# Kernel tuning notes

Measured on AMD Instinct MI355X. Metric: run time of the kernel, lower is better.

## Reference

```python
import jax, jax.numpy as jnp
import numpy as np

B, S, D, H = 2, 2048, 1024, 16
HD = D // H

def setup_inputs() -> dict:
    key = jax.random.key(0)
    k1, k2, k3 = jax.random.split(key, 3)
    x = jax.random.normal(k1, (B, S, D), dtype=jnp.float32)
    c_attn_w = jax.random.normal(k2, (D, 3 * D), dtype=jnp.float32) * 0.02
    c_attn_b = jnp.zeros((3 * D,), dtype=jnp.float32)
    c_proj_w = jax.random.normal(k3, (D, D), dtype=jnp.float32) * 0.02
    c_proj_b = jnp.zeros((D,), dtype=jnp.float32)
    return {"x": x, "c_attn_w": c_attn_w, "c_attn_b": c_attn_b,
            "c_proj_w": c_proj_w, "c_proj_b": c_proj_b}

def reference(x, c_attn_w, c_attn_b, c_proj_w, c_proj_b):
    bsz, seq_len, d = x.shape
    # Conv1D: addmm(bias, x, weight) -> x @ W + b
    qkv = x @ c_attn_w + c_attn_b                      # [B,S,3D]
    xq, xk, xv = jnp.split(qkv, 3, axis=-1)
    # [B,H,S,hd]
    xq = xq.reshape(bsz, seq_len, H, HD).transpose(0, 2, 1, 3)
    xk = xk.reshape(bsz, seq_len, H, HD).transpose(0, 2, 1, 3)
    xv = xv.reshape(bsz, seq_len, H, HD).transpose(0, 2, 1, 3)
    # Eager attention: QK^T / sqrt(hd), causal mask, softmax, AV
    scale = jnp.asarray(HD, x.dtype) ** 0.5
    attn_weights = jnp.einsum('bhqd,bhkd->bhqk', xq, xk) / scale
    causal = jnp.tril(jnp.ones((seq_len, seq_len), dtype=bool))
    mask_value = jnp.finfo(attn_weights.dtype).min
    attn_weights = jnp.where(causal[None, None], attn_weights, mask_value)
    attn_weights = jax.nn.softmax(attn_weights, axis=-1)
    attn_output = jnp.einsum('bhqk,bhkd->bhqd', attn_weights, xv)  # [B,H,S,hd]
    attn_output = attn_output.transpose(0, 2, 1, 3).reshape(bsz, seq_len, d)
    attn_output = attn_output @ c_proj_w + c_proj_b
    return attn_output
```

## Files before the change

### kernel.cpp

```cpp
#include <hip/hip_runtime.h>
#include <hip/hip_bf16.h>
#include <stdint.h>

#define S_LEN 2048
#define D_DIM 1024
#define N_HEAD 16

typedef unsigned short u16;
typedef __attribute__((ext_vector_type(4))) float f32x4;
typedef __attribute__((ext_vector_type(16))) float f32x16;
typedef __attribute__((ext_vector_type(8))) short bf16x8;
typedef __attribute__((ext_vector_type(4))) unsigned short u16x4;
typedef __attribute__((ext_vector_type(8))) unsigned short u16x8;
typedef __attribute__((ext_vector_type(4))) float flt4;

#define MFMA16(a, b, c) __builtin_amdgcn_mfma_f32_16x16x32_bf16((a), (b), (c), 0, 0, 0)
#define MFMA32(a, b, c) __builtin_amdgcn_mfma_f32_32x32x16_bf16((a), (b), (c), 0, 0, 0)

__device__ __forceinline__ u16 f32_bf16(float f) {
    union { float f; uint32_t u; } x;
    x.f = f;
    uint32_t r = (x.u + 0x7FFFu + ((x.u >> 16) & 1u)) >> 16;
    return (u16)r;
}

__device__ __forceinline__ uint32_t pack2(float a, float b) {
    __hip_bfloat162 h = __float22bfloat162_rn(float2{a, b});
    return *(uint32_t*)&h;
}

__device__ __forceinline__ void gload_lds16(const void* g, void* l) {
    __builtin_amdgcn_global_load_lds(
        (const __attribute__((address_space(1))) unsigned int*)(uintptr_t)g,
        (__attribute__((address_space(3))) unsigned int*)(uint32_t)(uintptr_t)l,
        16, 0, 0);
}


__global__ __launch_bounds__(256) void cvt_bf16_kernel(const float* __restrict__ in,
                                                       u16* __restrict__ out, int n) {
    int i = (blockIdx.x * 256 + threadIdx.x) * 4;
    if (i < n) {
        flt4 v = *(const flt4*)(in + i);
        u16x4 u;
        u[0] = f32_bf16(v[0]); u[1] = f32_bf16(v[1]);
        u[2] = f32_bf16(v[2]); u[3] = f32_bf16(v[3]);
        *(u16x4*)(out + i) = u;
    }
}

__global__ __launch_bounds__(256) void transpose_cvt_kernel(const float* __restrict__ in,
                                                            u16* __restrict__ out,
                                                            int R, int C) {
    __shared__ float tile[32][33];
    int tc = blockIdx.x * 32, tr = blockIdx.y * 32;
    int lx = threadIdx.x & 31, ly = threadIdx.x >> 5;
#pragma unroll
    for (int i = 0; i < 32; i += 8)
        tile[ly + i][lx] = in[(size_t)(tr + ly + i) * C + tc + lx];
    __syncthreads();
#pragma unroll
    for (int i = 0; i < 32; i += 8)
        out[(size_t)(tc + ly + i) * R + tr + lx] = f32_bf16(tile[lx][ly + i]);
}

__global__ __launch_bounds__(256) void v_transpose_kernel(const u16* __restrict__ Vin,
                                                          u16* __restrict__ Vt) {
    __shared__ u16 tile[64][72];
    const int bh = blockIdx.y, st = blockIdx.x;
    const int t = threadIdx.x;
    const u16* src = Vin + ((size_t)bh * S_LEN + st * 64) * 64;
    const int r = t >> 3, c = (t & 7) * 8;
#pragma unroll
    for (int i = 0; i < 2; i++) {
        int rr = r + i * 32;
        *(u16x8*)&tile[rr][c] = *(const u16x8*)(src + rr * 64 + c);
    }
    __syncthreads();
    const int d = t & 63, sc = t >> 6;
    u16x8 o0, o1;
#pragma unroll
    for (int j = 0; j < 8; j++) o0[j] = tile[sc * 16 + j][d];
#pragma unroll
    for (int j = 0; j < 8; j++) o1[j] = tile[sc * 16 + 8 + j][d];
    u16* dst = Vt + ((size_t)bh * 64 + d) * S_LEN + st * 64 + sc * 16;
    *(u16x8*)dst = o0;
    *(u16x8*)(dst + 8) = o1;
}


template <int MODE>
__global__ __launch_bounds__(256)
void gemm_bt_kernel(const u16* __restrict__ A, const u16* __restrict__ Bt,
                    const float* __restrict__ bias,
                    float* __restrict__ outF,
                    u16* __restrict__ qo, u16* __restrict__ ko, u16* __restrict__ vo,
                    int M, int N, int K) {
    __shared__ u16 As[128 * 32];
    __shared__ u16 Bs[128 * 32];
    const int tid = threadIdx.x;
    const int w = tid >> 6, lane = tid & 63;
    const int lr = lane & 15, lg = lane >> 4;
    const int gx = gridDim.x;
    const int nwg = gx * gridDim.y;
    const int wg = blockIdx.y * gx + blockIdx.x;
    const int swz = (wg & 7) * (nwg >> 3) + (wg >> 3);
    const int bm = (swz / gx) * 128, bn = (swz % gx) * 128;
    const int wr = w >> 1, wc = w & 1;

    f32x4 acc[4][4];
#pragma unroll
    for (int m = 0; m < 4; m++)
#pragma unroll
        for (int n = 0; n < 4; n++) acc[m][n] = (f32x4){0.f, 0.f, 0.f, 0.f};

    const u16* Abase = A + (size_t)(bm + (tid >> 2)) * K + (tid & 3) * 8;
    const u16* Bbase = Bt + (size_t)(bn + (tid >> 2)) * K + (tid & 3) * 8;
    u16* AsW = As + w * 512;
    u16* BsW = Bs + w * 512;

    for (int kt = 0; kt < K; kt += 32) {
        gload_lds16(Abase + kt, AsW);
        gload_lds16(Abase + kt + (size_t)64 * K, AsW + 2048);
        gload_lds16(Bbase + kt, BsW);
        gload_lds16(Bbase + kt + (size_t)64 * K, BsW + 2048);
        __syncthreads();

        bf16x8 a[4], b[4];
        const bf16x8* Av = (const bf16x8*)As;
        const bf16x8* Bv = (const bf16x8*)Bs;
#pragma unroll
        for (int m = 0; m < 4; m++) a[m] = Av[(wr * 64 + m * 16 + lr) * 4 + lg];
#pragma unroll
        for (int n = 0; n < 4; n++) b[n] = Bv[(wc * 64 + n * 16 + lr) * 4 + lg];
#pragma unroll
        for (int m = 0; m < 4; m++)
#pragma unroll
            for (int n = 0; n < 4; n++)
                acc[m][n] = MFMA16(a[m], b[n], acc[m][n]);
        __syncthreads();
    }

    const int rowb = bm + wr * 64, colb = bn + wc * 64;
    if (MODE == 0) {
#pragma unroll
        for (int m = 0; m < 4; m++)
#pragma unroll
            for (int j = 0; j < 4; j++) {
                int r = rowb + m * 16 + lg * 4 + j;
                size_t base = (size_t)r * N;
#pragma unroll
                for (int n = 0; n < 4; n++) {
                    int c = colb + n * 16 + lr;
                    outF[base + c] = acc[m][n][j] + bias[c];
                }
            }
    } else {
        const int part = colb >> 10;
        const int ccb = colb & (D_DIM - 1);
        u16* dst = (part == 0) ? qo : (part == 1) ? ko : vo;
        const float scale = (part == 0) ? 0.125f * 1.44269504f : 1.f;
#pragma unroll
        for (int m = 0; m < 4; m++)
#pragma unroll
            for (int j = 0; j < 4; j++) {
                int r = rowb + m * 16 + lg * 4 + j;
                int bb = r >> 11, s = r & (S_LEN - 1);
#pragma unroll
                for (int n = 0; n < 4; n++) {
                    int c = colb + n * 16 + lr;
                    int cc = ccb + n * 16 + lr;
                    int h = cc >> 6, d = cc & 63;
                    float v = (acc[m][n][j] + bias[c]) * scale;
                    dst[((size_t)(bb * N_HEAD + h) * S_LEN + s) * 64 + d] = f32_bf16(v);
                }
            }
    }
}


__global__ __launch_bounds__(128, 2)
void flash_attn_kernel(const u16* __restrict__ Qg, const u16* __restrict__ Kg,
                       const u16* __restrict__ Vt, u16* __restrict__ Og) {
    const int id = blockIdx.x;
    const int bh = id & 31;
    const int p  = id >> 5;
    const int w = threadIdx.x >> 6;
    const int lane = threadIdx.x & 63;
    const int ql = lane & 31, hi = lane >> 5;
    const int qbA = p * 32, qbB = (63 - p) * 32;
    const int last = 63 - p;

    const u16* Qh = Qg + (size_t)bh * S_LEN * 64;
    const u16* Kh = Kg + (size_t)bh * S_LEN * 64;
    const u16* Vh = Vt + (size_t)bh * 64 * S_LEN;

    __shared__ float mbuf[2][64][34];

    bf16x8 qfA[4], qfB[4];
#pragma unroll
    for (int c = 0; c < 4; c++) {
        qfA[c] = *(const bf16x8*)(Qh + (size_t)(qbA + ql) * 64 + c * 16 + hi * 8);
        qfB[c] = *(const bf16x8*)(Qh + (size_t)(qbB + ql) * 64 + c * 16 + hi * 8);
    }

    f32x16 otA0 = {}, otA1 = {}, otB0 = {}, otB1 = {};
    float mA = -1e30f, lA = 0.f, mB = -1e30f, lB = 0.f;

    auto loadKV = [&](int t, bf16x8 (&k)[4], bf16x8 (&v)[4]) {
        const u16* kp = Kh + ((size_t)t * 32 + ql) * 64 + hi * 8;
#pragma unroll
        for (int c = 0; c < 4; c++) k[c] = *(const bf16x8*)(kp + c * 16);
        const size_t kv0 = (size_t)t * 32;
#pragma unroll
        for (int u = 0; u < 4; u++)
            v[u] = *(const bf16x8*)(Vh + ((size_t)((u >> 1) * 32 + ql)) * S_LEN + kv0 + (u & 1) * 16 + hi * 8);
    };

    auto softpv = [&](const f32x16& st, bool diag, float& m, float& l,
                      f32x16& o0, f32x16& o1, const bf16x8 (&v)[4]) {
        float s[16];
#pragma unroll
        for (int r = 0; r < 16; r++) s[r] = st[r];
        if (diag) {
#pragma unroll
            for (int r = 0; r < 16; r++) {
                int kvl = ((r & 3) + 8 * (r >> 2)) + 4 * hi;
                if (kvl > ql) s[r] = -1e30f;
            }
        }
        float u0 = fmaxf(fmaxf(s[0], s[1]), s[2]);
        float u1 = fmaxf(fmaxf(s[3], s[4]), s[5]);
        float u2 = fmaxf(fmaxf(s[6], s[7]), s[8]);
        float u3 = fmaxf(fmaxf(s[9], s[10]), s[11]);
        float u4 = fmaxf(fmaxf(s[12], s[13]), s[14]);
        float tmax = fmaxf(fmaxf(fmaxf(u0, u1), u2), fmaxf(fmaxf(u3, u4), s[15]));
        tmax = fmaxf(tmax, __shfl_xor(tmax, 32));

        float corr = 1.f;
        if (!__all(tmax <= m + 11.5f)) {
            float mn = fmaxf(m, tmax);
            corr = __builtin_amdgcn_exp2f(m - mn);
            m = mn;
            o0 *= corr;
            o1 *= corr;
        }
        float pe[16];
        float rs = 0.f;
#pragma unroll
        for (int r = 0; r < 16; r++) { pe[r] = __builtin_amdgcn_exp2f(s[r] - m); rs += pe[r]; }
        rs += __shfl_xor(rs, 32);
        l = l * corr + rs;

        uint32_t wv[8];
#pragma unroll
        for (int sp = 0; sp < 8; sp++) wv[sp] = pack2(pe[2 * sp], pe[2 * sp + 1]);
        auto r02 = __builtin_amdgcn_permlane32_swap(wv[0], wv[2], false, false);
        auto r13 = __builtin_amdgcn_permlane32_swap(wv[1], wv[3], false, false);
        auto r46 = __builtin_amdgcn_permlane32_swap(wv[4], wv[6], false, false);
        auto r57 = __builtin_amdgcn_permlane32_swap(wv[5], wv[7], false, false);
        union { uint32_t u[4]; bf16x8 v; } pa0, pa1;
        pa0.u[0] = r02[0]; pa0.u[1] = r13[0]; pa0.u[2] = r02[1]; pa0.u[3] = r13[1];
        pa1.u[0] = r46[0]; pa1.u[1] = r57[0]; pa1.u[2] = r46[1]; pa1.u[3] = r57[1];

        __builtin_amdgcn_s_setprio(1);
        o0 = MFMA32(v[0], pa0.v, o0);
        o0 = MFMA32(v[1], pa1.v, o0);
        o1 = MFMA32(v[2], pa0.v, o1);
        o1 = MFMA32(v[3], pa1.v, o1);
        __builtin_amdgcn_s_setprio(0);
    };

    auto step = [&](int t, const bf16x8 (&k)[4], const bf16x8 (&v)[4]) {
        const bool actA = (t <= p);
        f32x16 stA = {}, stB = {};
        __builtin_amdgcn_s_setprio(1);
        if (actA) {
#pragma unroll
            for (int c = 0; c < 4; c++) stA = MFMA32(k[c], qfA[c], stA);
        }
#pragma unroll
        for (int c = 0; c < 4; c++) stB = MFMA32(k[c], qfB[c], stB);
        __builtin_amdgcn_s_setprio(0);
        if (actA) softpv(stA, t == p, mA, lA, otA0, otA1, v);
        softpv(stB, t == last, mB, lB, otB0, otB1, v);
    };

    bf16x8 k0[4], v0[4], k1[4], v1[4];
    loadKV(w, k0, v0);
    int t = w;
    for (;;) {
        if (t + 2 <= last) loadKV(t + 2, k1, v1);
        step(t, k0, v0);
        t += 2;
        if (t > last) break;
        if (t + 2 <= last) loadKV(t + 2, k0, v0);
        step(t, k1, v1);
        t += 2;
        if (t > last) break;
    }

    if (w == 1) {
        float* bA = mbuf[0][lane];
        float* bB = mbuf[1][lane];
        bA[0] = mA; bA[1] = lA;
        bB[0] = mB; bB[1] = lB;
#pragma unroll
        for (int r = 0; r < 16; r++) {
            bA[2 + r] = otA0[r]; bA[18 + r] = otA1[r];
            bB[2 + r] = otB0[r]; bB[18 + r] = otB1[r];
        }
    }
    __syncthreads();
    if (w == 0) {
        const int bb = bh >> 4, hh = bh & 15;
        auto fin = [&](float m0, float l0, const f32x16& o0, const f32x16& o1,
                       const float* b, int qbase) {
            float m1 = b[0], l1 = b[1];
            float ms = fmaxf(m0, m1);
            float a0 = __builtin_amdgcn_exp2f(m0 - ms);
            float a1 = __builtin_amdgcn_exp2f(m1 - ms);
            float inv = 1.f / (l0 * a0 + l1 * a1);
            u16* orow = Og + ((size_t)(bb * S_LEN) + qbase + ql) * D_DIM + hh * 64;
#pragma unroll
            for (int rp = 0; rp < 8; rp++) {
                int r = rp * 2;
                int d = ((r & 3) + 8 * (r >> 2)) + 4 * hi;
                float x0 = (o0[r] * a0 + b[2 + r] * a1) * inv;
                float x1 = (o0[r + 1] * a0 + b[2 + r + 1] * a1) * inv;
                *(uint32_t*)(orow + d) = pack2(x0, x1);
                float y0 = (o1[r] * a0 + b[18 + r] * a1) * inv;
                float y1 = (o1[r + 1] * a0 + b[18 + r + 1] * a1) * inv;
                *(uint32_t*)(orow + 32 + d) = pack2(y0, y1);
            }
        };
        fin(mA, lA, otA0, otA1, mbuf[0][lane], qbA);
        fin(mB, lB, otB0, otB1, mbuf[1][lane], qbB);
    }
}


extern "C" void kernel_launch(void* const* d_in, const int* in_sizes, int n_in,
                              void* d_out, int out_size, void* d_ws, size_t ws_size,
                              hipStream_t stream) {
    const float* x  = (const float*)d_in[0];
    const float* w1 = (const float*)d_in[1];
    const float* b1 = (const float*)d_in[2];
    const float* w2 = (const float*)d_in[3];
    const float* b2 = (const float*)d_in[4];
    float* out = (float*)d_out;

    u16* ws  = (u16*)d_ws;
    u16* xb  = ws;
    u16* w1t = xb  + 4096 * 1024;
    u16* w2t = w1t + 3072 * 1024;
    u16* q   = w2t + 1024 * 1024;
    u16* k   = q   + 4194304;
    u16* vt  = k   + 4194304;
    u16* x2  = vt  + 4194304;
    u16* v   = x2;

    cvt_bf16_kernel<<<dim3(4096), dim3(256), 0, stream>>>(x, xb, 4096 * 1024);
    transpose_cvt_kernel<<<dim3(3072 / 32, 1024 / 32), dim3(256), 0, stream>>>(w1, w1t, 1024, 3072);
    transpose_cvt_kernel<<<dim3(1024 / 32, 1024 / 32), dim3(256), 0, stream>>>(w2, w2t, 1024, 1024);

    gemm_bt_kernel<1><<<dim3(3072 / 128, 4096 / 128), dim3(256), 0, stream>>>(
        xb, w1t, b1, nullptr, q, k, v, 4096, 3072, 1024);

    v_transpose_kernel<<<dim3(S_LEN / 64, 32), dim3(256), 0, stream>>>(v, vt);

    flash_attn_kernel<<<dim3(1024), dim3(128), 0, stream>>>(q, k, vt, x2);

    gemm_bt_kernel<0><<<dim3(1024 / 128, 4096 / 128), dim3(256), 0, stream>>>(
        x2, w2t, b2, out, nullptr, nullptr, nullptr, 4096, 1024, 1024);
}
```

Baseline: 232.9 us.

## Fuse V transpose into QKV GEMM epilogue and swizzle GEMM LDS tiles

Removes the separate V transpose kernel by having the QKV GEMM epilogue write V directly in transposed [bh, d, s] layout. This avoids an extra launch and a round trip through global memory for V, at the cost of strided scattered stores in the epilogue. The GEMM also applies an XOR swizzle to the LDS chunk placement and to the fragment reads to reduce shared-memory bank conflicts.

```diff
diff --git a/kernel.cpp b/kernel.cpp
--- a/kernel.cpp
+++ b/kernel.cpp
@@ -11,7 +11,6 @@
 typedef __attribute__((ext_vector_type(16))) float f32x16;
 typedef __attribute__((ext_vector_type(8))) short bf16x8;
 typedef __attribute__((ext_vector_type(4))) unsigned short u16x4;
-typedef __attribute__((ext_vector_type(8))) unsigned short u16x8;
 typedef __attribute__((ext_vector_type(4))) float flt4;
 
 #define MFMA16(a, b, c) __builtin_amdgcn_mfma_f32_16x16x32_bf16((a), (b), (c), 0, 0, 0)
@@ -64,37 +63,13 @@
         out[(size_t)(tc + ly + i) * R + tr + lx] = f32_bf16(tile[lx][ly + i]);
 }
 
-__global__ __launch_bounds__(256) void v_transpose_kernel(const u16* __restrict__ Vin,
-                                                          u16* __restrict__ Vt) {
-    __shared__ u16 tile[64][72];
-    const int bh = blockIdx.y, st = blockIdx.x;
-    const int t = threadIdx.x;
-    const u16* src = Vin + ((size_t)bh * S_LEN + st * 64) * 64;
-    const int r = t >> 3, c = (t & 7) * 8;
-#pragma unroll
-    for (int i = 0; i < 2; i++) {
-        int rr = r + i * 32;
-        *(u16x8*)&tile[rr][c] = *(const u16x8*)(src + rr * 64 + c);
-    }
-    __syncthreads();
-    const int d = t & 63, sc = t >> 6;
-    u16x8 o0, o1;
-#pragma unroll
-    for (int j = 0; j < 8; j++) o0[j] = tile[sc * 16 + j][d];
-#pragma unroll
-    for (int j = 0; j < 8; j++) o1[j] = tile[sc * 16 + 8 + j][d];
-    u16* dst = Vt + ((size_t)bh * 64 + d) * S_LEN + st * 64 + sc * 16;
-    *(u16x8*)dst = o0;
-    *(u16x8*)(dst + 8) = o1;
-}
-
 
 template <int MODE>
 __global__ __launch_bounds__(256)
 void gemm_bt_kernel(const u16* __restrict__ A, const u16* __restrict__ Bt,
                     const float* __restrict__ bias,
                     float* __restrict__ outF,
-                    u16* __restrict__ qo, u16* __restrict__ ko, u16* __restrict__ vo,
+                    u16* __restrict__ qo, u16* __restrict__ ko, u16* __restrict__ vto,
                     int M, int N, int K) {
     __shared__ u16 As[128 * 32];
     __shared__ u16 Bs[128 * 32];
@@ -114,10 +89,21 @@
 #pragma unroll
         for (int n = 0; n < 4; n++) acc[m][n] = (f32x4){0.f, 0.f, 0.f, 0.f};
 
-    const u16* Abase = A + (size_t)(bm + (tid >> 2)) * K + (tid & 3) * 8;
-    const u16* Bbase = Bt + (size_t)(bn + (tid >> 2)) * K + (tid & 3) * 8;
+    const int srow = tid >> 2;
+    const int schunk = (tid & 3) ^ ((srow >> 1) & 3);
+    const u16* Abase = A + (size_t)(bm + srow) * K + schunk * 8;
+    const u16* Bbase = Bt + (size_t)(bn + srow) * K + schunk * 8;
     u16* AsW = As + w * 512;
     u16* BsW = Bs + w * 512;
+
+    int aoff[4], boff[4];
+#pragma unroll
+    for (int m = 0; m < 4; m++) {
+        int Ra = wr * 64 + m * 16 + lr;
+        aoff[m] = Ra * 32 + ((lg ^ ((Ra >> 1) & 3)) * 8);
+        int Rb = wc * 64 + m * 16 + lr;
+        boff[m] = Rb * 32 + ((lg ^ ((Rb >> 1) & 3)) * 8);
+    }
 
     for (int kt = 0; kt < K; kt += 32) {
         gload_lds16(Abase + kt, AsW);
@@ -127,12 +113,10 @@
         __syncthreads();
 
         bf16x8 a[4], b[4];
-        const bf16x8* Av = (const bf16x8*)As;
-        const bf16x8* Bv = (const bf16x8*)Bs;
-#pragma unroll
-        for (int m = 0; m < 4; m++) a[m] = Av[(wr * 64 + m * 16 + lr) * 4 + lg];
-#pragma unroll
-        for (int n = 0; n < 4; n++) b[n] = Bv[(wc * 64 + n * 16 + lr) * 4 + lg];
+#pragma unroll
+        for (int m = 0; m < 4; m++) a[m] = *(const bf16x8*)(As + aoff[m]);
+#pragma unroll
+        for (int n = 0; n < 4; n++) b[n] = *(const bf16x8*)(Bs + boff[n]);
 #pragma unroll
         for (int m = 0; m < 4; m++)
 #pragma unroll
@@ -158,23 +142,41 @@
     } else {
         const int part = colb >> 10;
         const int ccb = colb & (D_DIM - 1);
-        u16* dst = (part == 0) ? qo : (part == 1) ? ko : vo;
-        const float scale = (part == 0) ? 0.125f * 1.44269504f : 1.f;
-#pragma unroll
-        for (int m = 0; m < 4; m++)
-#pragma unroll
-            for (int j = 0; j < 4; j++) {
-                int r = rowb + m * 16 + lg * 4 + j;
-                int bb = r >> 11, s = r & (S_LEN - 1);
-#pragma unroll
-                for (int n = 0; n < 4; n++) {
-                    int c = colb + n * 16 + lr;
-                    int cc = ccb + n * 16 + lr;
-                    int h = cc >> 6, d = cc & 63;
-                    float v = (acc[m][n][j] + bias[c]) * scale;
-                    dst[((size_t)(bb * N_HEAD + h) * S_LEN + s) * 64 + d] = f32_bf16(v);
+        if (part < 2) {
+            u16* dst = (part == 0) ? qo : ko;
+            const float scale = (part == 0) ? 0.125f * 1.44269504f : 1.f;
+#pragma unroll
+            for (int m = 0; m < 4; m++)
+#pragma unroll
+                for (int j = 0; j < 4; j++) {
+                    int r = rowb + m * 16 + lg * 4 + j;
+                    int bb = r >> 11, s = r & (S_LEN - 1);
+#pragma unroll
+                    for (int n = 0; n < 4; n++) {
+                        int c = colb + n * 16 + lr;
+                        int cc = ccb + n * 16 + lr;
+                        int h = cc >> 6, d = cc & 63;
+                        float v = (acc[m][n][j] + bias[c]) * scale;
+                        dst[((size_t)(bb * N_HEAD + h) * S_LEN + s) * 64 + d] = f32_bf16(v);
+                    }
                 }
-            }
+        } else {
+#pragma unroll
+            for (int m = 0; m < 4; m++)
+#pragma unroll
+                for (int j = 0; j < 4; j++) {
+                    int r = rowb + m * 16 + lg * 4 + j;
+                    int bb = r >> 11, s = r & (S_LEN - 1);
+#pragma unroll
+                    for (int n = 0; n < 4; n++) {
+                        int c = colb + n * 16 + lr;
+                        int cc = ccb + n * 16 + lr;
+                        int h = cc >> 6, d = cc & 63;
+                        float v = acc[m][n][j] + bias[c];
+                        vto[((size_t)(bb * N_HEAD + h) * 64 + d) * S_LEN + s] = f32_bf16(v);
+                    }
+                }
+        }
     }
 }
 
@@ -358,16 +360,13 @@
     u16* k   = q   + 4194304;
     u16* vt  = k   + 4194304;
     u16* x2  = vt  + 4194304;
-    u16* v   = x2;
 
     cvt_bf16_kernel<<<dim3(4096), dim3(256), 0, stream>>>(x, xb, 4096 * 1024);
     transpose_cvt_kernel<<<dim3(3072 / 32, 1024 / 32), dim3(256), 0, stream>>>(w1, w1t, 1024, 3072);
     transpose_cvt_kernel<<<dim3(1024 / 32, 1024 / 32), dim3(256), 0, stream>>>(w2, w2t, 1024, 1024);
 
     gemm_bt_kernel<1><<<dim3(3072 / 128, 4096 / 128), dim3(256), 0, stream>>>(
-        xb, w1t, b1, nullptr, q, k, v, 4096, 3072, 1024);
-
-    v_transpose_kernel<<<dim3(S_LEN / 64, 32), dim3(256), 0, stream>>>(v, vt);
+        xb, w1t, b1, nullptr, q, k, vt, 4096, 3072, 1024);
 
     flash_attn_kernel<<<dim3(1024), dim3(128), 0, stream>>>(q, k, vt, x2);
 
```

Measured after the change: 225.8 us. 1.03x faster.
